# Optimization experiments

Hardware: AMD Instinct MI355X
Metric: run time of the kernel (lower is better)

Reference implementation:

```python
import jax, jax.numpy as jnp
from jax import lax
import numpy as np

B, T, IN, H, L = 4096, 1024, 2, 16, 3


def _lstm_layer(x_tbd, h0, c0, Wih, Whh, b):
    # x_tbd: [T, B, D_in]; returns hidden states [T, B, H]
    def step(carry, xt):
        h, c = carry
        g = xt @ Wih.T + h @ Whh.T + b  # [B, 4H], gate order i,f,g,o (PyTorch)
        i, f, gg, o = jnp.split(g, 4, axis=-1)
        i = jax.nn.sigmoid(i)
        f = jax.nn.sigmoid(f)
        gg = jnp.tanh(gg)
        o = jax.nn.sigmoid(o)
        c = f * c + i * gg
        h = o * jnp.tanh(c)
        return (h, c), h

    _, hs = lax.scan(step, (h0, c0), x_tbd)
    return hs


def setup_inputs() -> dict:
    key = jax.random.key(0)
    ks = jax.random.split(key, 16)

    def xavier(k, shape):
        fan_out, fan_in = shape
        s = jnp.sqrt(6.0 / (fan_in + fan_out)).astype(jnp.float32)
        return jax.random.uniform(k, shape, jnp.float32, -1.0, 1.0) * s

    inp = {
        "x": jax.random.normal(ks[0], (B, T, IN), jnp.float32),
        "h0": jax.random.normal(ks[1], (L, B, H), jnp.float32) * 0.1,
        "c0": jax.random.normal(ks[2], (L, B, H), jnp.float32) * 0.1,
        "W_ih0": xavier(ks[3], (4 * H, IN)),
        "W_hh0": xavier(ks[4], (4 * H, H)),
        "b_ih0": jnp.zeros((4 * H,), jnp.float32),
        "b_hh0": jnp.zeros((4 * H,), jnp.float32),
        "W_ih1": xavier(ks[5], (4 * H, H)),
        "W_hh1": xavier(ks[6], (4 * H, H)),
        "b_ih1": jnp.zeros((4 * H,), jnp.float32),
        "b_hh1": jnp.zeros((4 * H,), jnp.float32),
        "W_ih2": xavier(ks[7], (4 * H, H)),
        "W_hh2": xavier(ks[8], (4 * H, H)),
        "b_ih2": jnp.zeros((4 * H,), jnp.float32),
        "b_hh2": jnp.zeros((4 * H,), jnp.float32),
        "W_fc": xavier(ks[9], (1, H)),
        "b_fc": jnp.zeros((1,), jnp.float32),
    }
    return inp


def reference(x, h0, c0, W_ih0, W_hh0, b_ih0, b_hh0, W_ih1, W_hh1, b_ih1, b_hh1,
              W_ih2, W_hh2, b_ih2, b_hh2, W_fc, b_fc):
    layers = [
        (W_ih0, W_hh0, b_ih0 + b_hh0),
        (W_ih1, W_hh1, b_ih1 + b_hh1),
        (W_ih2, W_hh2, b_ih2 + b_hh2),
    ]
    h = jnp.transpose(x, (1, 0, 2))  # [T, B, IN]
    for l, (Wih, Whh, b) in enumerate(layers):
        h = _lstm_layer(h, h0[l], c0[l], Wih, Whh, b)  # [T, B, H]
    last = h[-1]  # [B, H] == out[:, -1, :]
    return last @ W_fc.T + b_fc  # [B, 1]
```

## Files before the change

kernel.cpp:

```cpp
#include <hip/hip_runtime.h>

#define NB 4096
#define NT 1024

typedef float f2 __attribute__((ext_vector_type(2)));
typedef float f4 __attribute__((ext_vector_type(4)));

#define GATE(accv, creg, hout) {                                              \
    float e_ = __builtin_amdgcn_exp2f((accv) * kpre);                         \
    float r_ = __builtin_amdgcn_rcpf(1.0f + e_);                              \
    float a_ = fmaf(r_, kA, kB);                                              \
    int ai_ = __float_as_int(a_);                                             \
    float iv_ = __int_as_float(__builtin_amdgcn_mov_dpp(ai_, 0x00, 0xF, 0xF, 0)); \
    float fv_ = __int_as_float(__builtin_amdgcn_mov_dpp(ai_, 0x55, 0xF, 0xF, 0)); \
    float gv_ = __int_as_float(__builtin_amdgcn_mov_dpp(ai_, 0xAA, 0xF, 0xF, 0)); \
    float ov_ = __int_as_float(__builtin_amdgcn_mov_dpp(ai_, 0xFF, 0xF, 0xF, 0)); \
    creg = fmaf(fv_, creg, iv_ * gv_);                                        \
    float e2_ = __builtin_amdgcn_exp2f(creg * -2.88539008177792681f);         \
    float r2_ = __builtin_amdgcn_rcpf(1.0f + e2_);                            \
    hout = ov_ * fmaf(r2_, 2.0f, -1.0f);                                      \
}

#define HSUM4(v) (((v).x + (v).y) + ((v).z + (v).w))

__global__ __launch_bounds__(256, 3) void lstm3_kernel(
    const float* __restrict__ x,
    const float* __restrict__ h0,
    const float* __restrict__ c0,
    const float* __restrict__ Wih0, const float* __restrict__ Whh0,
    const float* __restrict__ bih0, const float* __restrict__ bhh0,
    const float* __restrict__ Wih1, const float* __restrict__ Whh1,
    const float* __restrict__ bih1, const float* __restrict__ bhh1,
    const float* __restrict__ Wih2, const float* __restrict__ Whh2,
    const float* __restrict__ bih2, const float* __restrict__ bhh2,
    const float* __restrict__ Wfc,  const float* __restrict__ bfc,
    float* __restrict__ out)
{
    __shared__ float ldsH[3][4][16];
    __shared__ float ldsX[4][64];

    const int lane = threadIdx.x & 63;
    const int wv   = threadIdx.x >> 6;
    const int b    = (blockIdx.x << 2) + wv;
    const int q    = lane >> 2;
    const int g    = lane & 3;
    const int row  = g * 16 + q;

    const float kpre = (g == 2) ? -2.88539008177792681f : -1.44269504088896340f;
    const float kA   = (g == 2) ? 2.0f : 1.0f;
    const float kB   = (g == 2) ? -1.0f : 0.0f;

    f2 wi0 = *(const f2*)&Wih0[row * 2];
    f4 wh0[4], wi1[4], wh1[4], wi2[4], wh2[4];
#pragma unroll
    for (int k = 0; k < 4; ++k) {
        wh0[k] = *(const f4*)&Whh0[row * 16 + 4 * k];
        wi1[k] = *(const f4*)&Wih1[row * 16 + 4 * k];
        wh1[k] = *(const f4*)&Whh1[row * 16 + 4 * k];
        wi2[k] = *(const f4*)&Wih2[row * 16 + 4 * k];
        wh2[k] = *(const f4*)&Whh2[row * 16 + 4 * k];
    }
    const float bias0 = bih0[row] + bhh0[row];
    const float bias1 = bih1[row] + bhh1[row];
    const float bias2 = bih2[row] + bhh2[row];

    float c0r = c0[0 * NB * 16 + b * 16 + q];
    float c1r = c0[1 * NB * 16 + b * 16 + q];
    float c2r = c0[2 * NB * 16 + b * 16 + q];
    if (lane < 16) {
        ldsH[0][wv][lane] = h0[0 * NB * 16 + b * 16 + lane];
        ldsH[1][wv][lane] = h0[1 * NB * 16 + b * 16 + lane];
        ldsH[2][wv][lane] = h0[2 * NB * 16 + b * 16 + lane];
    }
    __builtin_amdgcn_wave_barrier();

    const f4* __restrict__ hb0 = (const f4*)&ldsH[0][wv][0];
    const f4* __restrict__ hb1 = (const f4*)&ldsH[1][wv][0];
    const f4* __restrict__ hb2 = (const f4*)&ldsH[2][wv][0];
    const f2* __restrict__ xb  = (const f2*)&ldsX[wv][0];

    float xpre = x[(size_t)b * (NT * 2) + lane];

    for (int ch = 0; ch < (NT * 2) / 64; ++ch) {
        ldsX[wv][lane] = xpre;
        __builtin_amdgcn_wave_barrier();
        if (ch + 1 < (NT * 2) / 64)
            xpre = x[(size_t)b * (NT * 2) + (ch + 1) * 64 + lane];

#pragma unroll 2
        for (int s = 0; s < 32; ++s) {
            const f2 x2 = xb[s];

            f4 ha = hb0[0], hc = hb0[1], hd = hb0[2], he = hb0[3];
            f4 a0 = wh0[0] * ha;
            f4 a1 = wh0[1] * hc;
            a0 = wh0[2] * hd + a0;
            a1 = wh0[3] * he + a1;
            a0 = a0 + a1;
            float acc = HSUM4(a0) + fmaf(wi0.x, x2.x, fmaf(wi0.y, x2.y, bias0));
            float hn0;
            GATE(acc, c0r, hn0);
            if (g == 0) ldsH[0][wv][q] = hn0;
            __builtin_amdgcn_wave_barrier();

            ha = hb1[0]; hc = hb1[1]; hd = hb1[2]; he = hb1[3];
            f4 xa = hb0[0], xc = hb0[1], xd = hb0[2], xe = hb0[3];
            a0 = wh1[0] * ha;
            a1 = wh1[1] * hc;
            f4 a2 = wh1[2] * hd;
            f4 a3 = wh1[3] * he;
            a0 = wi1[0] * xa + a0;
            a1 = wi1[1] * xc + a1;
            a2 = wi1[2] * xd + a2;
            a3 = wi1[3] * xe + a3;
            a0 = (a0 + a1) + (a2 + a3);
            acc = HSUM4(a0) + bias1;
            float hn1;
            GATE(acc, c1r, hn1);
            if (g == 0) ldsH[1][wv][q] = hn1;
            __builtin_amdgcn_wave_barrier();

            ha = hb2[0]; hc = hb2[1]; hd = hb2[2]; he = hb2[3];
            xa = hb1[0]; xc = hb1[1]; xd = hb1[2]; xe = hb1[3];
            a0 = wh2[0] * ha;
            a1 = wh2[1] * hc;
            a2 = wh2[2] * hd;
            a3 = wh2[3] * he;
            a0 = wi2[0] * xa + a0;
            a1 = wi2[1] * xc + a1;
            a2 = wi2[2] * xd + a2;
            a3 = wi2[3] * xe + a3;
            a0 = (a0 + a1) + (a2 + a3);
            acc = HSUM4(a0) + bias2;
            float hn2;
            GATE(acc, c2r, hn2);
            if (g == 0) ldsH[2][wv][q] = hn2;
            __builtin_amdgcn_wave_barrier();
        }
    }

    if (lane == 0) {
        float s = bfc[0];
#pragma unroll
        for (int k = 0; k < 16; ++k) s = fmaf(ldsH[2][wv][k], Wfc[k], s);
        out[b] = s;
    }
}

extern "C" void kernel_launch(void* const* d_in, const int* in_sizes, int n_in,
                              void* d_out, int out_size, void* d_ws, size_t ws_size,
                              hipStream_t stream) {
    (void)in_sizes; (void)n_in; (void)d_ws; (void)ws_size; (void)out_size;
    const float* x    = (const float*)d_in[0];
    const float* h0   = (const float*)d_in[1];
    const float* c0   = (const float*)d_in[2];
    const float* Wih0 = (const float*)d_in[3];
    const float* Whh0 = (const float*)d_in[4];
    const float* bih0 = (const float*)d_in[5];
    const float* bhh0 = (const float*)d_in[6];
    const float* Wih1 = (const float*)d_in[7];
    const float* Whh1 = (const float*)d_in[8];
    const float* bih1 = (const float*)d_in[9];
    const float* bhh1 = (const float*)d_in[10];
    const float* Wih2 = (const float*)d_in[11];
    const float* Whh2 = (const float*)d_in[12];
    const float* bih2 = (const float*)d_in[13];
    const float* bhh2 = (const float*)d_in[14];
    const float* Wfc  = (const float*)d_in[15];
    const float* bfc  = (const float*)d_in[16];
    float* out = (float*)d_out;

    lstm3_kernel<<<NB / 4, 256, 0, stream>>>(
        x, h0, c0, Wih0, Whh0, bih0, bhh0, Wih1, Whh1, bih1, bhh1,
        Wih2, Whh2, bih2, bhh2, Wfc, bfc, out);
}
```

Baseline: 1.106 ms.

## Process two batch sequences per wave to interleave independent recurrences

Each wave now handles two batch elements (b and b+2048), running both independent LSTM chains at every layer and time step and sharing the wave barriers. The grid is halved and launch bounds drop to 2 blocks per SM. The aim is instruction-level parallelism that hides the latency of the serial recurrence (LDS reads, exp/rcp, DPP) within one wave, in exchange for more registers and fewer waves in flight. Unrolling of the inner step loop is reduced to 1.

```diff
diff --git a/kernel.cpp b/kernel.cpp
--- a/kernel.cpp
+++ b/kernel.cpp
@@ -2,6 +2,7 @@
 
 #define NB 4096
 #define NT 1024
+#define NWAVE 2048
 
 typedef float f2 __attribute__((ext_vector_type(2)));
 typedef float f4 __attribute__((ext_vector_type(4)));
@@ -23,7 +24,37 @@
 
 #define HSUM4(v) (((v).x + (v).y) + ((v).z + (v).w))
 
-__global__ __launch_bounds__(256, 3) void lstm3_kernel(
+#define HB(L, p, k) (*(const f4*)&ldsH[L][wv][p][4 * (k)])
+
+#define L0(p, x2, c, hn) {                                                    \
+    f4 h0_ = HB(0, p, 0), h1_ = HB(0, p, 1), h2_ = HB(0, p, 2), h3_ = HB(0, p, 3); \
+    f4 a0_ = wh0[0] * h0_;                                                    \
+    f4 a1_ = wh0[1] * h1_;                                                    \
+    a0_ = wh0[2] * h2_ + a0_;                                                 \
+    a1_ = wh0[3] * h3_ + a1_;                                                 \
+    a0_ = a0_ + a1_;                                                          \
+    float acc_ = HSUM4(a0_) + fmaf(wi0.x, (x2).x, fmaf(wi0.y, (x2).y, bias0)); \
+    GATE(acc_, c, hn);                                                        \
+}
+
+#define LN(L, p, wh, wi, bias, c, hn) {                                       \
+    f4 h0_ = HB(L, p, 0), h1_ = HB(L, p, 1), h2_ = HB(L, p, 2), h3_ = HB(L, p, 3); \
+    f4 x0_ = HB((L) - 1, p, 0), x1_ = HB((L) - 1, p, 1);                      \
+    f4 x2_ = HB((L) - 1, p, 2), x3_ = HB((L) - 1, p, 3);                      \
+    f4 a0_ = wh[0] * h0_;                                                     \
+    f4 a1_ = wh[1] * h1_;                                                     \
+    f4 a2_ = wh[2] * h2_;                                                     \
+    f4 a3_ = wh[3] * h3_;                                                     \
+    a0_ = wi[0] * x0_ + a0_;                                                  \
+    a1_ = wi[1] * x1_ + a1_;                                                  \
+    a2_ = wi[2] * x2_ + a2_;                                                  \
+    a3_ = wi[3] * x3_ + a3_;                                                  \
+    a0_ = (a0_ + a1_) + (a2_ + a3_);                                          \
+    float acc_ = HSUM4(a0_) + bias;                                           \
+    GATE(acc_, c, hn);                                                        \
+}
+
+__global__ __launch_bounds__(256, 2) void lstm3_kernel(
     const float* __restrict__ x,
     const float* __restrict__ h0,
     const float* __restrict__ c0,
@@ -36,12 +67,14 @@
     const float* __restrict__ Wfc,  const float* __restrict__ bfc,
     float* __restrict__ out)
 {
-    __shared__ float ldsH[3][4][16];
-    __shared__ float ldsX[4][64];
+    __shared__ float ldsH[3][4][2][16];
+    __shared__ float ldsX[4][2][64];
 
     const int lane = threadIdx.x & 63;
     const int wv   = threadIdx.x >> 6;
-    const int b    = (blockIdx.x << 2) + wv;
+    const int wg   = (blockIdx.x << 2) + wv;
+    const int bA   = wg;
+    const int bB   = wg + NWAVE;
     const int q    = lane >> 2;
     const int g    = lane & 3;
     const int row  = g * 16 + q;
@@ -64,86 +97,81 @@
     const float bias1 = bih1[row] + bhh1[row];
     const float bias2 = bih2[row] + bhh2[row];
 
-    float c0r = c0[0 * NB * 16 + b * 16 + q];
-    float c1r = c0[1 * NB * 16 + b * 16 + q];
-    float c2r = c0[2 * NB * 16 + b * 16 + q];
+    float cA0 = c0[0 * NB * 16 + bA * 16 + q];
+    float cA1 = c0[1 * NB * 16 + bA * 16 + q];
+    float cA2 = c0[2 * NB * 16 + bA * 16 + q];
+    float cB0 = c0[0 * NB * 16 + bB * 16 + q];
+    float cB1 = c0[1 * NB * 16 + bB * 16 + q];
+    float cB2 = c0[2 * NB * 16 + bB * 16 + q];
     if (lane < 16) {
-        ldsH[0][wv][lane] = h0[0 * NB * 16 + b * 16 + lane];
-        ldsH[1][wv][lane] = h0[1 * NB * 16 + b * 16 + lane];
-        ldsH[2][wv][lane] = h0[2 * NB * 16 + b * 16 + lane];
+#pragma unroll
+        for (int l = 0; l < 3; ++l) {
+            ldsH[l][wv][0][lane] = h0[l * NB * 16 + bA * 16 + lane];
+            ldsH[l][wv][1][lane] = h0[l * NB * 16 + bB * 16 + lane];
+        }
     }
     __builtin_amdgcn_wave_barrier();
 
-    const f4* __restrict__ hb0 = (const f4*)&ldsH[0][wv][0];
-    const f4* __restrict__ hb1 = (const f4*)&ldsH[1][wv][0];
-    const f4* __restrict__ hb2 = (const f4*)&ldsH[2][wv][0];
-    const f2* __restrict__ xb  = (const f2*)&ldsX[wv][0];
-
-    float xpre = x[(size_t)b * (NT * 2) + lane];
+    const f2* __restrict__ xbA = (const f2*)&ldsX[wv][0][0];
+    const f2* __restrict__ xbB = (const f2*)&ldsX[wv][1][0];
+
+    const float* xgA = x + (size_t)bA * (NT * 2);
+    const float* xgB = x + (size_t)bB * (NT * 2);
+    float xpreA = xgA[lane];
+    float xpreB = xgB[lane];
 
     for (int ch = 0; ch < (NT * 2) / 64; ++ch) {
-        ldsX[wv][lane] = xpre;
+        ldsX[wv][0][lane] = xpreA;
+        ldsX[wv][1][lane] = xpreB;
         __builtin_amdgcn_wave_barrier();
-        if (ch + 1 < (NT * 2) / 64)
-            xpre = x[(size_t)b * (NT * 2) + (ch + 1) * 64 + lane];
-
-#pragma unroll 2
+        if (ch + 1 < (NT * 2) / 64) {
+            xpreA = xgA[(ch + 1) * 64 + lane];
+            xpreB = xgB[(ch + 1) * 64 + lane];
+        }
+
+#pragma unroll 1
         for (int s = 0; s < 32; ++s) {
-            const f2 x2 = xb[s];
-
-            f4 ha = hb0[0], hc = hb0[1], hd = hb0[2], he = hb0[3];
-            f4 a0 = wh0[0] * ha;
-            f4 a1 = wh0[1] * hc;
-            a0 = wh0[2] * hd + a0;
-            a1 = wh0[3] * he + a1;
-            a0 = a0 + a1;
-            float acc = HSUM4(a0) + fmaf(wi0.x, x2.x, fmaf(wi0.y, x2.y, bias0));
-            float hn0;
-            GATE(acc, c0r, hn0);
-            if (g == 0) ldsH[0][wv][q] = hn0;
+            const f2 x2A = xbA[s];
+            const f2 x2B = xbB[s];
+
+            float hn0A, hn0B;
+            L0(0, x2A, cA0, hn0A);
+            L0(1, x2B, cB0, hn0B);
+            if (g == 0) {
+                ldsH[0][wv][0][q] = hn0A;
+                ldsH[0][wv][1][q] = hn0B;
+            }
             __builtin_amdgcn_wave_barrier();
 
-            ha = hb1[0]; hc = hb1[1]; hd = hb1[2]; he = hb1[3];
-            f4 xa = hb0[0], xc = hb0[1], xd = hb0[2], xe = hb0[3];
-            a0 = wh1[0] * ha;
-            a1 = wh1[1] * hc;
-            f4 a2 = wh1[2] * hd;
-            f4 a3 = wh1[3] * he;
-            a0 = wi1[0] * xa + a0;
-            a1 = wi1[1] * xc + a1;
-            a2 = wi1[2] * xd + a2;
-            a3 = wi1[3] * xe + a3;
-            a0 = (a0 + a1) + (a2 + a3);
-            acc = HSUM4(a0) + bias1;
-            float hn1;
-            GATE(acc, c1r, hn1);
-            if (g == 0) ldsH[1][wv][q] = hn1;
+            float hn1A, hn1B;
+            LN(1, 0, wh1, wi1, bias1, cA1, hn1A);
+            LN(1, 1, wh1, wi1, bias1, cB1, hn1B);
+            if (g == 0) {
+                ldsH[1][wv][0][q] = hn1A;
+                ldsH[1][wv][1][q] = hn1B;
+            }
             __builtin_amdgcn_wave_barrier();
 
-            ha = hb2[0]; hc = hb2[1]; hd = hb2[2]; he = hb2[3];
-            xa = hb1[0]; xc = hb1[1]; xd = hb1[2]; xe = hb1[3];
-            a0 = wh2[0] * ha;
-            a1 = wh2[1] * hc;
-            a2 = wh2[2] * hd;
-            a3 = wh2[3] * he;
-            a0 = wi2[0] * xa + a0;
-            a1 = wi2[1] * xc + a1;
-            a2 = wi2[2] * xd + a2;
-            a3 = wi2[3] * xe + a3;
-            a0 = (a0 + a1) + (a2 + a3);
-            acc = HSUM4(a0) + bias2;
-            float hn2;
-            GATE(acc, c2r, hn2);
-            if (g == 0) ldsH[2][wv][q] = hn2;
+            float hn2A, hn2B;
+            LN(2, 0, wh2, wi2, bias2, cA2, hn2A);
+            LN(2, 1, wh2, wi2, bias2, cB2, hn2B);
+            if (g == 0) {
+                ldsH[2][wv][0][q] = hn2A;
+                ldsH[2][wv][1][q] = hn2B;
+            }
             __builtin_amdgcn_wave_barrier();
         }
     }
 
     if (lane == 0) {
-        float s = bfc[0];
+        float sA = bfc[0], sB = bfc[0];
 #pragma unroll
-        for (int k = 0; k < 16; ++k) s = fmaf(ldsH[2][wv][k], Wfc[k], s);
-        out[b] = s;
+        for (int k = 0; k < 16; ++k) {
+            sA = fmaf(ldsH[2][wv][0][k], Wfc[k], sA);
+            sB = fmaf(ldsH[2][wv][1][k], Wfc[k], sB);
+        }
+        out[bA] = sA;
+        out[bB] = sB;
     }
 }
 
@@ -170,7 +198,7 @@
     const float* bfc  = (const float*)d_in[16];
     float* out = (float*)d_out;
 
-    lstm3_kernel<<<NB / 4, 256, 0, stream>>>(
+    lstm3_kernel<<<NWAVE / 4, 256, 0, stream>>>(
         x, h0, c0, Wih0, Whh0, bih0, bhh0, Wih1, Whh1, bih1, bhh1,
         Wih2, Whh2, bih2, bhh2, Wfc, bfc, out);
 }
```

Measured after the change: 1.189 ms. 1.07x slower.
